# Performance work log

Hardware: AMD Instinct MI355X
Metric: run time of the kernel (lower is better)

## Reference

```python
import jax, jax.numpy as jnp
import numpy as np

N_NODES = 100000
N_EDGES = 1600000
N_GRAPHS = 1024


def gcn_conv(x, W, b, src, dst, n_nodes):
    """PyG-style GCNConv: add self-loops, symmetric deg^-1/2 normalization,
    linear transform, scatter-add aggregation, bias."""
    h = x @ W  # [N, out]
    ones = jnp.ones(src.shape[0], dtype=h.dtype)
    deg = jax.ops.segment_sum(ones, dst, num_segments=n_nodes) + 1.0  # +1 self-loop
    dinv = jax.lax.rsqrt(deg)  # deg^-1/2, deg >= 1 so safe
    norm = dinv[src] * dinv[dst]  # [E]
    msg = h[src] * norm[:, None]  # gather + scale
    agg = jax.ops.segment_sum(msg, dst, num_segments=n_nodes)  # scatter-add
    # self-loop contribution: norm_ii = dinv_i^2
    return agg + h * (dinv * dinv)[:, None] + b


def setup_inputs() -> dict:
    key = jax.random.key(0)
    ks = jax.random.split(key, 12)
    x = jax.random.normal(ks[0], (N_NODES, 5), dtype=jnp.float32)
    src = jax.random.randint(ks[1], (N_EDGES,), 0, N_NODES)
    dst = jax.random.randint(ks[2], (N_EDGES,), 0, N_NODES)
    batch = jnp.sort(jax.random.randint(ks[3], (N_NODES,), 0, N_GRAPHS))
    def glorot(k, shp):
        lim = float(np.sqrt(6.0 / (shp[0] + shp[1])))
        return jax.random.uniform(k, shp, jnp.float32, -lim, lim)
    return {
        "x": x, "src": src, "dst": dst, "batch": batch,
        "W1": glorot(ks[4], (5, 16)),  "b1": jnp.zeros((16,), jnp.float32),
        "W2": glorot(ks[5], (16, 32)), "b2": jnp.zeros((32,), jnp.float32),
        "W3": glorot(ks[6], (32, 64)), "b3": jnp.zeros((64,), jnp.float32),
        "Wfc": glorot(ks[7], (64, 2)), "bfc": jnp.zeros((2,), jnp.float32),
    }


def reference(x, src, dst, batch, W1, b1, W2, b2, W3, b3, Wfc, bfc):
    h = jax.nn.relu(gcn_conv(x, W1, b1, src, dst, N_NODES))
    h = jax.nn.relu(gcn_conv(h, W2, b2, src, dst, N_NODES))
    h = jax.nn.relu(gcn_conv(h, W3, b3, src, dst, N_NODES))
    # global mean pool over graphs
    summed = jax.ops.segment_sum(h, batch, num_segments=N_GRAPHS)  # [G, 64]
    counts = jax.ops.segment_sum(jnp.ones(h.shape[0], h.dtype), batch, num_segments=N_GRAPHS)
    pooled = summed / jnp.maximum(counts, 1.0)[:, None]
    logits = pooled @ Wfc + bfc  # [G, 2]
    return jax.nn.log_softmax(logits, axis=1)
```

## Files before the change

### kernel.cpp

```cpp
#include <hip/hip_runtime.h>


#define BLK 256
#define CH 4096
#define EPT (CH / BLK)
#define NB 256
#define GSH 9
#define GSZ 512


__device__ inline float bfu_lo(unsigned int w) { return __uint_as_float(w << 16); }
__device__ inline float bfu_hi(unsigned int w) { return __uint_as_float(w & 0xffff0000u); }
__device__ inline unsigned int f2bf(float f) {
    unsigned int w = __float_as_uint(f);
    return (w + 0x7fffu + ((w >> 16) & 1u)) >> 16;
}
__device__ inline unsigned int pack2(float a, float b) {
    return f2bf(a) | (f2bf(b) << 16);
}


__global__ void hist1_kernel(const int* __restrict__ dst, int* __restrict__ cnt,
                             int E, int nChunks) {
    __shared__ int h[NB];
    int t = threadIdx.x, b = blockIdx.x;
    h[t] = 0;
    __syncthreads();
    int base = b * CH;
#pragma unroll
    for (int j = 0; j < EPT; ++j) {
        int e = base + j * BLK + t;
        if (e < E) atomicAdd(&h[dst[e] >> GSH], 1);
    }
    __syncthreads();
    cnt[(size_t)t * nChunks + b] = h[t];
}

__global__ void seg_scan_kernel(int* __restrict__ cnt, int* __restrict__ bucketTot,
                                int nChunks) {
    __shared__ int part[256];
    int b = blockIdx.x, t = threadIdx.x;
    size_t base = (size_t)b * nChunks;
    int per = (nChunks + 255) / 256;
    int lo = t * per, hi = lo + per < nChunks ? lo + per : nChunks;
    int sum = 0;
    for (int i = lo; i < hi; ++i) sum += cnt[base + i];
    part[t] = sum;
    __syncthreads();
    for (int off = 1; off < 256; off <<= 1) {
        int x = (t >= off) ? part[t - off] : 0;
        __syncthreads();
        if (t >= off) part[t] += x;
        __syncthreads();
    }
    int run = part[t] - sum;
    for (int i = lo; i < hi; ++i) { int v = cnt[base + i]; cnt[base + i] = run; run += v; }
    if (t == 255) bucketTot[b] = part[255];
}

__global__ void bucket_scan_kernel(const int* __restrict__ bucketTot,
                                   int* __restrict__ groupBeg, int E) {
    __shared__ int part[256];
    int t = threadIdx.x;
    int v = bucketTot[t];
    part[t] = v;
    __syncthreads();
    for (int off = 1; off < 256; off <<= 1) {
        int x = (t >= off) ? part[t - off] : 0;
        __syncthreads();
        if (t >= off) part[t] += x;
        __syncthreads();
    }
    groupBeg[t] = part[t] - v;
    if (t == 0) groupBeg[NB] = E;
}

__global__ void scatter1_kernel(const int* __restrict__ src, const int* __restrict__ dst,
                                const int* __restrict__ cnt, const int* __restrict__ groupBeg,
                                int* __restrict__ pe, int E, int nChunks) {
    __shared__ int offs[NB];
    int t = threadIdx.x, b = blockIdx.x;
    offs[t] = cnt[(size_t)t * nChunks + b] + groupBeg[t];
    __syncthreads();
    int base = b * CH;
#pragma unroll
    for (int j = 0; j < EPT; ++j) {
        int e = base + j * BLK + t;
        if (e < E) {
            int d = dst[e];
            int p = atomicAdd(&offs[d >> GSH], 1);
            pe[p] = ((d & (GSZ - 1)) << 17) | src[e];
        }
    }
}


__global__ void group_csr_kernel(const int* __restrict__ pe, const int* __restrict__ groupBeg,
                                 int* __restrict__ col, int* __restrict__ row_ptr,
                                 float* __restrict__ dinv, const float* __restrict__ x,
                                 uint4* __restrict__ xa, int N, int E) {
    __shared__ int hist[GSZ];
    __shared__ int scn[GSZ];
    __shared__ int part[256];
    int g = blockIdx.x, t = threadIdx.x;
    hist[t] = 0; hist[t + 256] = 0;
    __syncthreads();
    int lo = groupBeg[g], hi = groupBeg[g + 1];
    for (int e = lo + t; e < hi; e += BLK)
        atomicAdd(&hist[pe[e] >> 17], 1);
    __syncthreads();
    int a0 = hist[2 * t], a1 = hist[2 * t + 1];
    int s2 = a0 + a1;
    part[t] = s2;
    __syncthreads();
    for (int off = 1; off < 256; off <<= 1) {
        int xx = (t >= off) ? part[t - off] : 0;
        __syncthreads();
        if (t >= off) part[t] += xx;
        __syncthreads();
    }
    int excl = part[t] - s2;
    scn[2 * t] = excl;
    scn[2 * t + 1] = excl + a0;
    __syncthreads();
#pragma unroll
    for (int i = t; i < GSZ; i += BLK) {
        int d = (g << GSH) + i;
        if (d < N) {
            row_ptr[d] = lo + scn[i];
            float di = rsqrtf((float)hist[i] + 1.0f);
            dinv[d] = di;
            const float* r = x + (size_t)d * 5;
            uint4 u;
            u.x = pack2(r[0] * di, r[1] * di);
            u.y = pack2(r[2] * di, r[3] * di);
            u.z = pack2(r[4] * di, 0.f);
            u.w = 0u;
            xa[d] = u;
        }
    }
    if (g == 0 && t == 0) row_ptr[N] = E;
    __syncthreads();
    hist[t] = scn[t]; hist[t + 256] = scn[t + 256];
    __syncthreads();
    for (int e = lo + t; e < hi; e += BLK) {
        int v = pe[e];
        int p = atomicAdd(&hist[v >> 17], 1);
        col[lo + p] = v & 0x1FFFF;
    }
}


template <int F, int FIN, int FOUT, int CAP, bool PRESCALE_OUT>
__global__ void fused_layer_kernel(const int* __restrict__ row_ptr, const int* __restrict__ col,
                                   const uint4* __restrict__ xb, const float* __restrict__ W,
                                   const float* __restrict__ bias, const float* __restrict__ dinv,
                                   uint2* __restrict__ outb, int N) {
    constexpr int TPN = F / 8;
    constexpr int NPB = 256 / TPN;
    constexpr int RQ  = F / 8;
    constexpr int QO  = FOUT / 4;
    constexpr int STR = F + 1;
    __shared__ int lcol[CAP];
    __shared__ int lrp[NPB + 1];
    __shared__ float dl[NPB];
    __shared__ __align__(16) float gl[NPB * STR];
    __shared__ __align__(16) float wl[FIN * FOUT];
    __shared__ __align__(16) float bl[FOUT];
    int t = threadIdx.x;
    int n0 = blockIdx.x * NPB;
    for (int i = t; i <= NPB; i += 256) lrp[i] = row_ptr[min(n0 + i, N)];
    for (int i = t; i < NPB; i += 256) dl[i] = dinv[min(n0 + i, N - 1)];
    for (int i = t; i < FIN * FOUT / 4; i += 256)
        ((float4*)wl)[i] = ((const float4*)W)[i];
    for (int i = t; i < FOUT; i += 256) bl[i] = bias[i];
    __syncthreads();
    int base = lrp[0];
    int total = lrp[NPB] - base;
    int stage = total < CAP ? total : CAP;
    for (int i = t; i < stage; i += 256) lcol[i] = col[base + i];
    __syncthreads();
    {
        int ln = t / TPN, q = t % TPN;
        int n = n0 + ln;
        if (n < N) {
            float acc[8];
            uint4 u = xb[(size_t)n * RQ + q];
            acc[0] = bfu_lo(u.x); acc[1] = bfu_hi(u.x);
            acc[2] = bfu_lo(u.y); acc[3] = bfu_hi(u.y);
            acc[4] = bfu_lo(u.z); acc[5] = bfu_hi(u.z);
            acc[6] = bfu_lo(u.w); acc[7] = bfu_hi(u.w);
            int beg = lrp[ln] - base, end = lrp[ln + 1] - base;
            int stop = end < stage ? end : stage;
            int e = beg;
            for (; e + 7 < stop; e += 8) {
                uint4 uu[8];
#pragma unroll
                for (int j = 0; j < 8; ++j) uu[j] = xb[(size_t)lcol[e + j] * RQ + q];
#pragma unroll
                for (int j = 0; j < 8; ++j) {
                    acc[0] += bfu_lo(uu[j].x); acc[1] += bfu_hi(uu[j].x);
                    acc[2] += bfu_lo(uu[j].y); acc[3] += bfu_hi(uu[j].y);
                    acc[4] += bfu_lo(uu[j].z); acc[5] += bfu_hi(uu[j].z);
                    acc[6] += bfu_lo(uu[j].w); acc[7] += bfu_hi(uu[j].w);
                }
            }
            for (; e + 3 < stop; e += 4) {
                uint4 uu[4];
#pragma unroll
                for (int j = 0; j < 4; ++j) uu[j] = xb[(size_t)lcol[e + j] * RQ + q];
#pragma unroll
                for (int j = 0; j < 4; ++j) {
                    acc[0] += bfu_lo(uu[j].x); acc[1] += bfu_hi(uu[j].x);
                    acc[2] += bfu_lo(uu[j].y); acc[3] += bfu_hi(uu[j].y);
                    acc[4] += bfu_lo(uu[j].z); acc[5] += bfu_hi(uu[j].z);
                    acc[6] += bfu_lo(uu[j].w); acc[7] += bfu_hi(uu[j].w);
                }
            }
            for (; e < end; ++e) {
                int s = (e < stage) ? lcol[e] : col[base + e];
                uint4 uu = xb[(size_t)s * RQ + q];
                acc[0] += bfu_lo(uu.x); acc[1] += bfu_hi(uu.x);
                acc[2] += bfu_lo(uu.y); acc[3] += bfu_hi(uu.y);
                acc[4] += bfu_lo(uu.z); acc[5] += bfu_hi(uu.z);
                acc[6] += bfu_lo(uu.w); acc[7] += bfu_hi(uu.w);
            }
            float* gr = gl + ln * STR + q * 8;
#pragma unroll
            for (int j = 0; j < 8; ++j) gr[j] = acc[j];
        }
    }
    __syncthreads();
    for (int task = t; task < NPB * QO; task += 256) {
        int ln2 = task / QO, qq = task % QO;
        int n2 = n0 + ln2;
        if (n2 >= N) continue;
        float di = dl[ln2];
        const float* row = gl + ln2 * STR;
        float4 acc = make_float4(0.f, 0.f, 0.f, 0.f);
#pragma unroll
        for (int k = 0; k < FIN; ++k) {
            float rk = row[k];
            float4 wk = *(const float4*)(wl + k * FOUT + 4 * qq);
            acc.x = fmaf(rk, wk.x, acc.x);
            acc.y = fmaf(rk, wk.y, acc.y);
            acc.z = fmaf(rk, wk.z, acc.z);
            acc.w = fmaf(rk, wk.w, acc.w);
        }
        float4 bq = *(const float4*)(bl + 4 * qq);
        float4 v;
        v.x = fmaxf(di * acc.x + bq.x, 0.f);
        v.y = fmaxf(di * acc.y + bq.y, 0.f);
        v.z = fmaxf(di * acc.z + bq.z, 0.f);
        v.w = fmaxf(di * acc.w + bq.w, 0.f);
        if (PRESCALE_OUT) { v.x *= di; v.y *= di; v.z *= di; v.w *= di; }
        uint2 o;
        o.x = pack2(v.x, v.y);
        o.y = pack2(v.z, v.w);
        outb[(size_t)n2 * QO + qq] = o;
    }
}


__global__ void bounds_kernel(const int* __restrict__ batch, int* __restrict__ start,
                              int N, int G) {
    int g = blockIdx.x * blockDim.x + threadIdx.x;
    if (g > G) return;
    if (g == G) { start[G] = N; return; }
    int lo = 0, hi = N;
    while (lo < hi) {
        int mid = (lo + hi) >> 1;
        if (batch[mid] < g) lo = mid + 1; else hi = mid;
    }
    start[g] = lo;
}

__global__ void pool_head_kernel(const unsigned int* __restrict__ h, const int* __restrict__ start,
                                 const float* __restrict__ Wfc, const float* __restrict__ bfc,
                                 float* __restrict__ out) {
    __shared__ float part[8][64];
    int g = blockIdx.x;
    int t = threadIdx.x;
    int u = t & 31, w = t >> 5;
    int s = start[g], e = start[g + 1];
    float a0 = 0.f, a1 = 0.f;
    for (int n = s + w; n < e; n += 8) {
        unsigned int word = h[(size_t)n * 32 + u];
        a0 += bfu_lo(word);
        a1 += bfu_hi(word);
    }
    part[w][2 * u]     = a0;
    part[w][2 * u + 1] = a1;
    __syncthreads();
    if (t < 64) {
        float p = 0.f;
#pragma unroll
        for (int w2 = 0; w2 < 8; ++w2) p += part[w2][t];
        p /= fmaxf((float)(e - s), 1.0f);
        float l0 = p * Wfc[t * 2 + 0];
        float l1 = p * Wfc[t * 2 + 1];
#pragma unroll
        for (int off = 32; off; off >>= 1) {
            l0 += __shfl_down(l0, off);
            l1 += __shfl_down(l1, off);
        }
        if (t == 0) {
            l0 += bfc[0]; l1 += bfc[1];
            float m   = fmaxf(l0, l1);
            float lse = m + logf(expf(l0 - m) + expf(l1 - m));
            out[g * 2 + 0] = l0 - lse;
            out[g * 2 + 1] = l1 - lse;
        }
    }
}


extern "C" void kernel_launch(void* const* d_in, const int* in_sizes, int n_in,
                              void* d_out, int out_size, void* d_ws, size_t ws_size,
                              hipStream_t stream) {
    const float* x     = (const float*)d_in[0];
    const int*   src   = (const int*)d_in[1];
    const int*   dst   = (const int*)d_in[2];
    const int*   batch = (const int*)d_in[3];
    const float* W1    = (const float*)d_in[4];
    const float* b1    = (const float*)d_in[5];
    const float* W2    = (const float*)d_in[6];
    const float* b2    = (const float*)d_in[7];
    const float* W3    = (const float*)d_in[8];
    const float* b3    = (const float*)d_in[9];
    const float* Wfc   = (const float*)d_in[10];
    const float* bfc   = (const float*)d_in[11];
    float* out = (float*)d_out;

    const int N = in_sizes[0] / 5;
    const int E = in_sizes[1];
    const int G = out_size / 2;

    const int nChunks = (E + CH - 1) / CH;
    const int M       = NB * nChunks;
    const int Mpad    = (M + 3) & ~3;
    const int nGroups = (N + GSZ - 1) / GSZ;

    int* row_ptr  = (int*)d_ws;
    int* col      = row_ptr + N + 4;
    int* cnt      = col + E;
    int* groupBeg = cnt + Mpad;
    int* bucketTot= groupBeg + 260;
    int* start    = bucketTot + 256;
    float* dinv   = (float*)(start + G + 8);
    int*   Xa     = (int*)(dinv + N);
    int*   Xb     = Xa + (size_t)N * 16;
    int*   H3b    = Xb + (size_t)N * 8;
    int*   pe     = H3b;

    auto blocks = [](long n) { return (int)((n + BLK - 1) / BLK); };

    hist1_kernel<<<nChunks, 256, 0, stream>>>(dst, cnt, E, nChunks);
    seg_scan_kernel<<<NB, 256, 0, stream>>>(cnt, bucketTot, nChunks);
    bucket_scan_kernel<<<1, 256, 0, stream>>>(bucketTot, groupBeg, E);
    scatter1_kernel<<<nChunks, 256, 0, stream>>>(src, dst, cnt, groupBeg, pe, E, nChunks);
    group_csr_kernel<<<nGroups, 256, 0, stream>>>(pe, groupBeg, col, row_ptr, dinv,
                                                  x, (uint4*)Xa, N, E);

    bounds_kernel<<<blocks(G + 1), BLK, 0, stream>>>(batch, start, N, G);

    fused_layer_kernel<8, 5, 16, 6144, true><<<(N + 255) / 256, 256, 0, stream>>>(
        row_ptr, col, (const uint4*)Xa, W1, b1, dinv, (uint2*)Xb, N);

    fused_layer_kernel<16, 16, 32, 4096, true><<<(N + 127) / 128, 256, 0, stream>>>(
        row_ptr, col, (const uint4*)Xb, W2, b2, dinv, (uint2*)Xa, N);

    fused_layer_kernel<32, 32, 64, 2048, false><<<(N + 63) / 64, 256, 0, stream>>>(
        row_ptr, col, (const uint4*)Xa, W3, b3, dinv, (uint2*)H3b, N);

    pool_head_kernel<<<G, 256, 0, stream>>>((const unsigned int*)H3b, start, Wfc, bfc, out);
}
```

Before: 129.2 us.

## Fuse layer-3 GCN with global mean pooling via shared-memory atomics

Layer 3 now accumulates its ReLU outputs straight into per-graph pooled sums. It uses block-local shared-memory atomics for up to four graphs and global atomics otherwise, so the layer-3 hidden tensor is never written to memory or re-read. The pooling kernel becomes a small head kernel, and the bounds kernel also zeroes the pooled buffer. Shared-memory edge staging capacities are lowered for all three layers, probably to raise occupancy. The trade-off is float atomics, which make summation order nondeterministic, and more global atomic traffic when a block spans many graphs.

```diff
diff --git a/kernel.cpp b/kernel.cpp
--- a/kernel.cpp
+++ b/kernel.cpp
@@ -262,55 +262,175 @@
 }
 
 
-__global__ void bounds_kernel(const int* __restrict__ batch, int* __restrict__ start,
-                              int N, int G) {
-    int g = blockIdx.x * blockDim.x + threadIdx.x;
-    if (g > G) return;
-    if (g == G) { start[G] = N; return; }
+template <int CAP>
+__global__ void fused_layer3_pool_kernel(const int* __restrict__ row_ptr,
+                                         const int* __restrict__ col,
+                                         const uint4* __restrict__ xb,
+                                         const float* __restrict__ W,
+                                         const float* __restrict__ bias,
+                                         const float* __restrict__ dinv,
+                                         const int* __restrict__ batch,
+                                         float* __restrict__ pooled, int N) {
+    constexpr int F = 32, FIN = 32, FOUT = 64;
+    constexpr int TPN = 4, NPB = 64, RQ = 4, QO = 16, STR = 33;
+    __shared__ int lcol[CAP];
+    __shared__ int lrp[NPB + 1];
+    __shared__ float dl[NPB];
+    __shared__ int gbv[NPB];
+    __shared__ float pool_l[4][FOUT];
+    __shared__ __align__(16) float gl[NPB * STR];
+    __shared__ __align__(16) float wl[FIN * FOUT];
+    __shared__ __align__(16) float bl[FOUT];
+    int t = threadIdx.x;
+    int n0 = blockIdx.x * NPB;
+    for (int i = t; i <= NPB; i += 256) lrp[i] = row_ptr[min(n0 + i, N)];
+    for (int i = t; i < NPB; i += 256) {
+        int nn = min(n0 + i, N - 1);
+        dl[i] = dinv[nn];
+        gbv[i] = batch[nn];
+    }
+    for (int i = t; i < FIN * FOUT / 4; i += 256)
+        ((float4*)wl)[i] = ((const float4*)W)[i];
+    for (int i = t; i < FOUT; i += 256) bl[i] = bias[i];
+    if (t < 4 * FOUT) pool_l[t >> 6][t & 63] = 0.f;
+    __syncthreads();
+    int gfirst = gbv[0];
+    int base = lrp[0];
+    int total = lrp[NPB] - base;
+    int stage = total < CAP ? total : CAP;
+    for (int i = t; i < stage; i += 256) lcol[i] = col[base + i];
+    __syncthreads();
+    {
+        int ln = t / TPN, q = t % TPN;
+        int n = n0 + ln;
+        if (n < N) {
+            float acc[8];
+            uint4 u = xb[(size_t)n * RQ + q];
+            acc[0] = bfu_lo(u.x); acc[1] = bfu_hi(u.x);
+            acc[2] = bfu_lo(u.y); acc[3] = bfu_hi(u.y);
+            acc[4] = bfu_lo(u.z); acc[5] = bfu_hi(u.z);
+            acc[6] = bfu_lo(u.w); acc[7] = bfu_hi(u.w);
+            int beg = lrp[ln] - base, end = lrp[ln + 1] - base;
+            int stop = end < stage ? end : stage;
+            int e = beg;
+            for (; e + 7 < stop; e += 8) {
+                uint4 uu[8];
+#pragma unroll
+                for (int j = 0; j < 8; ++j) uu[j] = xb[(size_t)lcol[e + j] * RQ + q];
+#pragma unroll
+                for (int j = 0; j < 8; ++j) {
+                    acc[0] += bfu_lo(uu[j].x); acc[1] += bfu_hi(uu[j].x);
+                    acc[2] += bfu_lo(uu[j].y); acc[3] += bfu_hi(uu[j].y);
+                    acc[4] += bfu_lo(uu[j].z); acc[5] += bfu_hi(uu[j].z);
+                    acc[6] += bfu_lo(uu[j].w); acc[7] += bfu_hi(uu[j].w);
+                }
+            }
+            for (; e + 3 < stop; e += 4) {
+                uint4 uu[4];
+#pragma unroll
+                for (int j = 0; j < 4; ++j) uu[j] = xb[(size_t)lcol[e + j] * RQ + q];
+#pragma unroll
+                for (int j = 0; j < 4; ++j) {
+                    acc[0] += bfu_lo(uu[j].x); acc[1] += bfu_hi(uu[j].x);
+                    acc[2] += bfu_lo(uu[j].y); acc[3] += bfu_hi(uu[j].y);
+                    acc[4] += bfu_lo(uu[j].z); acc[5] += bfu_hi(uu[j].z);
+                    acc[6] += bfu_lo(uu[j].w); acc[7] += bfu_hi(uu[j].w);
+                }
+            }
+            for (; e < end; ++e) {
+                int s = (e < stage) ? lcol[e] : col[base + e];
+                uint4 uu = xb[(size_t)s * RQ + q];
+                acc[0] += bfu_lo(uu.x); acc[1] += bfu_hi(uu.x);
+                acc[2] += bfu_lo(uu.y); acc[3] += bfu_hi(uu.y);
+                acc[4] += bfu_lo(uu.z); acc[5] += bfu_hi(uu.z);
+                acc[6] += bfu_lo(uu.w); acc[7] += bfu_hi(uu.w);
+            }
+            float* gr = gl + ln * STR + q * 8;
+#pragma unroll
+            for (int j = 0; j < 8; ++j) gr[j] = acc[j];
+        }
+    }
+    __syncthreads();
+    for (int task = t; task < NPB * QO; task += 256) {
+        int ln2 = task >> 4, qq = task & 15;
+        int n2 = n0 + ln2;
+        if (n2 >= N) continue;
+        float di = dl[ln2];
+        const float* row = gl + ln2 * STR;
+        float4 acc = make_float4(0.f, 0.f, 0.f, 0.f);
+#pragma unroll
+        for (int k = 0; k < FIN; ++k) {
+            float rk = row[k];
+            float4 wk = *(const float4*)(wl + k * FOUT + 4 * qq);
+            acc.x = fmaf(rk, wk.x, acc.x);
+            acc.y = fmaf(rk, wk.y, acc.y);
+            acc.z = fmaf(rk, wk.z, acc.z);
+            acc.w = fmaf(rk, wk.w, acc.w);
+        }
+        float4 bq = *(const float4*)(bl + 4 * qq);
+        float4 v;
+        v.x = fmaxf(di * acc.x + bq.x, 0.f);
+        v.y = fmaxf(di * acc.y + bq.y, 0.f);
+        v.z = fmaxf(di * acc.z + bq.z, 0.f);
+        v.w = fmaxf(di * acc.w + bq.w, 0.f);
+        int gi = gbv[ln2] - gfirst;
+        if (gi < 4) {
+            atomicAdd(&pool_l[gi][4 * qq + 0], v.x);
+            atomicAdd(&pool_l[gi][4 * qq + 1], v.y);
+            atomicAdd(&pool_l[gi][4 * qq + 2], v.z);
+            atomicAdd(&pool_l[gi][4 * qq + 3], v.w);
+        } else {
+            float* pg = pooled + (size_t)gbv[ln2] * 64 + 4 * qq;
+            atomicAdd(pg + 0, v.x); atomicAdd(pg + 1, v.y);
+            atomicAdd(pg + 2, v.z); atomicAdd(pg + 3, v.w);
+        }
+    }
+    __syncthreads();
+    int glast = gbv[min(NPB, N - n0) - 1];
+    int ng = glast - gfirst + 1;
+    if (ng > 4) ng = 4;
+    for (int i = t; i < ng * FOUT; i += 256)
+        atomicAdd(&pooled[(size_t)(gfirst + (i >> 6)) * 64 + (i & 63)], pool_l[i >> 6][i & 63]);
+}
+
+
+__global__ void bounds_zero_kernel(const int* __restrict__ batch, int* __restrict__ start,
+                                   float* __restrict__ pooled, int N, int G) {
+    int idx = blockIdx.x * blockDim.x + threadIdx.x;
+    if (idx < G * 64) pooled[idx] = 0.f;
+    if (idx > G) return;
+    if (idx == G) { start[G] = N; return; }
     int lo = 0, hi = N;
     while (lo < hi) {
         int mid = (lo + hi) >> 1;
-        if (batch[mid] < g) lo = mid + 1; else hi = mid;
-    }
-    start[g] = lo;
-}
-
-__global__ void pool_head_kernel(const unsigned int* __restrict__ h, const int* __restrict__ start,
-                                 const float* __restrict__ Wfc, const float* __restrict__ bfc,
-                                 float* __restrict__ out) {
-    __shared__ float part[8][64];
-    int g = blockIdx.x;
+        if (batch[mid] < idx) lo = mid + 1; else hi = mid;
+    }
+    start[idx] = lo;
+}
+
+
+__global__ void head_kernel(const float* __restrict__ pooled, const int* __restrict__ start,
+                            const float* __restrict__ Wfc, const float* __restrict__ bfc,
+                            float* __restrict__ out, int G) {
     int t = threadIdx.x;
-    int u = t & 31, w = t >> 5;
-    int s = start[g], e = start[g + 1];
-    float a0 = 0.f, a1 = 0.f;
-    for (int n = s + w; n < e; n += 8) {
-        unsigned int word = h[(size_t)n * 32 + u];
-        a0 += bfu_lo(word);
-        a1 += bfu_hi(word);
-    }
-    part[w][2 * u]     = a0;
-    part[w][2 * u + 1] = a1;
-    __syncthreads();
-    if (t < 64) {
-        float p = 0.f;
-#pragma unroll
-        for (int w2 = 0; w2 < 8; ++w2) p += part[w2][t];
-        p /= fmaxf((float)(e - s), 1.0f);
-        float l0 = p * Wfc[t * 2 + 0];
-        float l1 = p * Wfc[t * 2 + 1];
-#pragma unroll
-        for (int off = 32; off; off >>= 1) {
-            l0 += __shfl_down(l0, off);
-            l1 += __shfl_down(l1, off);
-        }
-        if (t == 0) {
-            l0 += bfc[0]; l1 += bfc[1];
-            float m   = fmaxf(l0, l1);
-            float lse = m + logf(expf(l0 - m) + expf(l1 - m));
-            out[g * 2 + 0] = l0 - lse;
-            out[g * 2 + 1] = l1 - lse;
-        }
+    int g = blockIdx.x * 4 + (t >> 6);
+    int f = t & 63;
+    if (g >= G) return;
+    float cnt = (float)(start[g + 1] - start[g]);
+    float p = pooled[(size_t)g * 64 + f] / fmaxf(cnt, 1.0f);
+    float l0 = p * Wfc[f * 2 + 0];
+    float l1 = p * Wfc[f * 2 + 1];
+#pragma unroll
+    for (int off = 32; off; off >>= 1) {
+        l0 += __shfl_down(l0, off);
+        l1 += __shfl_down(l1, off);
+    }
+    if (f == 0) {
+        l0 += bfc[0]; l1 += bfc[1];
+        float m   = fmaxf(l0, l1);
+        float lse = m + logf(expf(l0 - m) + expf(l1 - m));
+        out[g * 2 + 0] = l0 - lse;
+        out[g * 2 + 1] = l1 - lse;
     }
 }
 
@@ -347,13 +467,15 @@
     int* groupBeg = cnt + Mpad;
     int* bucketTot= groupBeg + 260;
     int* start    = bucketTot + 256;
-    float* dinv   = (float*)(start + G + 8);
+    float* pooled = (float*)(start + G + 8);
+    float* dinv   = pooled + (size_t)G * 64;
     int*   Xa     = (int*)(dinv + N);
     int*   Xb     = Xa + (size_t)N * 16;
-    int*   H3b    = Xb + (size_t)N * 8;
-    int*   pe     = H3b;
+    int*   pe     = Xb + (size_t)N * 8;
 
     auto blocks = [](long n) { return (int)((n + BLK - 1) / BLK); };
+
+    bounds_zero_kernel<<<blocks((long)G * 64), BLK, 0, stream>>>(batch, start, pooled, N, G);
 
     hist1_kernel<<<nChunks, 256, 0, stream>>>(dst, cnt, E, nChunks);
     seg_scan_kernel<<<NB, 256, 0, stream>>>(cnt, bucketTot, nChunks);
@@ -362,16 +484,14 @@
     group_csr_kernel<<<nGroups, 256, 0, stream>>>(pe, groupBeg, col, row_ptr, dinv,
                                                   x, (uint4*)Xa, N, E);
 
-    bounds_kernel<<<blocks(G + 1), BLK, 0, stream>>>(batch, start, N, G);
-
-    fused_layer_kernel<8, 5, 16, 6144, true><<<(N + 255) / 256, 256, 0, stream>>>(
+    fused_layer_kernel<8, 5, 16, 5120, true><<<(N + 255) / 256, 256, 0, stream>>>(
         row_ptr, col, (const uint4*)Xa, W1, b1, dinv, (uint2*)Xb, N);
 
-    fused_layer_kernel<16, 16, 32, 4096, true><<<(N + 127) / 128, 256, 0, stream>>>(
+    fused_layer_kernel<16, 16, 32, 3072, true><<<(N + 127) / 128, 256, 0, stream>>>(
         row_ptr, col, (const uint4*)Xb, W2, b2, dinv, (uint2*)Xa, N);
 
-    fused_layer_kernel<32, 32, 64, 2048, false><<<(N + 63) / 64, 256, 0, stream>>>(
-        row_ptr, col, (const uint4*)Xa, W3, b3, dinv, (uint2*)H3b, N);
-
-    pool_head_kernel<<<G, 256, 0, stream>>>((const unsigned int*)H3b, start, Wfc, bfc, out);
-}
+    fused_layer3_pool_kernel<1536><<<(N + 63) / 64, 256, 0, stream>>>(
+        row_ptr, col, (const uint4*)Xa, W3, b3, dinv, batch, pooled, N);
+
+    head_kernel<<<(G + 3) / 4, 256, 0, stream>>>(pooled, start, Wfc, bfc, out, G);
+}
```

After: 158.3 us. +22.6%, slower.
